# Kernel optimization log

Hardware: AMD Instinct MI355X
Metric: run time of the kernel (lower is better)

The kernel has to match this reference:

```python
import jax, jax.numpy as jnp
import numpy as np

MODES = 2
LC = 4
N = 6000
KNN = 10
NODES = 64
CH = MODES ** 2
M = N * 2 * (KNN + 1)  # total candidate couplings


def setup_inputs() -> dict:
    key = jax.random.key(0)
    ks = jax.random.split(key, 6)
    return {
        "CK_inputs": jax.random.normal(ks[0], (N, 2 * (KNN + 1), 3), dtype=jnp.float32),
        "W_in": jax.random.normal(ks[1], (3, NODES), dtype=jnp.float32) * 0.1,
        "b_in": jnp.zeros((NODES,), dtype=jnp.float32),
        "W_hid": jax.random.normal(ks[2], (LC - 1, NODES, NODES), dtype=jnp.float32) * 0.1,
        "b_hid": jnp.zeros((LC - 1, NODES), dtype=jnp.float32),
        "W_out": jax.random.normal(ks[3], (NODES, CH), dtype=jnp.float32) * 0.1,
        "b_out": jnp.zeros((CH,), dtype=jnp.float32),
        "coo": jax.random.randint(ks[4], (2, M), 0, N, dtype=jnp.int32),
    }


def _mlp(x, W_in, b_in, W_hid, b_hid, W_out, b_out):
    # MLP: 3 -> 64, (LC-1) hidden 64->64 layers, 64 -> CH; ReLU activations.
    h = jax.nn.relu(x @ W_in + b_in)
    for i in range(W_hid.shape[0]):  # small fixed layer count
        h = jax.nn.relu(h @ W_hid[i] + b_hid[i])
    return h @ W_out + b_out  # [M, CH]


def reference(CK_inputs, W_in, b_in, W_hid, b_hid, W_out, b_out, coo):
    C_stripped = _mlp(CK_inputs.reshape(-1, 3), W_in, b_in, W_hid, b_hid, W_out, b_out)  # [M, CH]
    D = MODES * N
    # Original: for channel ch = mi*MODES+mj, scatter C_stripped[:, ch] at indices coo*MODES+mj
    # (mj added to BOTH row and col, replicating the source exactly). Indices are
    # independent of mi, so sum over mi first, then one scatter-add per mj.
    vals = C_stripped.reshape(-1, MODES, MODES).sum(axis=1)  # [M, MODES]; axis1=mi, axis2=mj
    dense = jnp.zeros((D, D), dtype=CK_inputs.dtype)
    for mj in range(MODES):
        idx = coo * MODES + mj  # [2, M]
        dense = dense.at[idx[0], idx[1]].add(vals[:, mj])
    return dense
```

## Files before the change

### kernel.cpp

```cpp
#include <hip/hip_runtime.h>
#include <stdint.h>

#define NN    6000
#define KNNC  10
#define MM    (NN * 2 * (KNNC + 1))
#define DD    (2 * NN)
#define LCH   3
#define BLK   256

#define FBLOCKS ((MM + 63) / 64)
#define NV      ((long long)DD * DD / 4)

__global__ __launch_bounds__(BLK) void fused_mlp_zero(
    const float* __restrict__ CK,
    const float* __restrict__ Win,
    const float* __restrict__ bin,
    const float* __restrict__ Whid,
    const float* __restrict__ bhid,
    const float* __restrict__ Wout,
    const float* __restrict__ bout,
    float* __restrict__ vals,
    float* __restrict__ out)
{
    const int tid  = threadIdx.x;
    const int wave = tid >> 6;
    const int lane = tid & 63;
    const int mlpw = blockIdx.x & 3;

    if (wave != mlpw) {
        const int fw = wave - (wave > mlpw ? 1 : 0);
        const long long ft = (long long)blockIdx.x * 192 + fw * 64 + lane;
        const long long stride = (long long)FBLOCKS * 192;
        float4 z = make_float4(0.f, 0.f, 0.f, 0.f);
        float4* outv = (float4*)out;
        for (long long i = ft; i < NV; i += stride) outv[i] = z;
        return;
    }

    const int m = blockIdx.x * 64 + lane;
    if (m >= MM) return;

    const float x0 = CK[m * 3 + 0];
    const float x1 = CK[m * 3 + 1];
    const float x2 = CK[m * 3 + 2];

    float h[64];
#pragma unroll
    for (int j = 0; j < 64; j++) {
        float a = bin[j];
        a = fmaf(x0, Win[j],       a);
        a = fmaf(x1, Win[64 + j],  a);
        a = fmaf(x2, Win[128 + j], a);
        h[j] = fmaxf(a, 0.0f);
    }

#pragma unroll 1
    for (int l = 0; l < LCH; l++) {
        const float4* __restrict__ W4 = (const float4*)(Whid + (l << 12));
        const float*  __restrict__ bh = bhid + (l << 6);
        float g[64];
#pragma unroll
        for (int j = 0; j < 64; j++) g[j] = bh[j];
#pragma unroll 8
        for (int k = 0; k < 64; k++) {
            const float hk = h[k];
            const float4* __restrict__ Wk = W4 + (k << 4);
#pragma unroll
            for (int j4 = 0; j4 < 16; j4++) {
                float4 w = Wk[j4];
                g[j4 * 4 + 0] = fmaf(w.x, hk, g[j4 * 4 + 0]);
                g[j4 * 4 + 1] = fmaf(w.y, hk, g[j4 * 4 + 1]);
                g[j4 * 4 + 2] = fmaf(w.z, hk, g[j4 * 4 + 2]);
                g[j4 * 4 + 3] = fmaf(w.w, hk, g[j4 * 4 + 3]);
            }
        }
#pragma unroll
        for (int j = 0; j < 64; j++) h[j] = fmaxf(g[j], 0.0f);
    }

    float v0 = bout[0] + bout[2];
    float v1 = bout[1] + bout[3];
#pragma unroll
    for (int k = 0; k < 64; k++) {
        float4 wo = *((const float4*)Wout + k);
        v0 = fmaf(h[k], wo.x + wo.z, v0);
        v1 = fmaf(h[k], wo.y + wo.w, v1);
    }
    vals[m * 2 + 0] = v0;
    vals[m * 2 + 1] = v1;
}

__global__ __launch_bounds__(BLK) void scatter_add(
    const float* __restrict__ vals,
    const int* __restrict__ coo,
    float* __restrict__ out)
{
    const int t = blockIdx.x * BLK + threadIdx.x;
    if (t >= MM) return;
    const int r2 = coo[t] * 2;
    const int c2 = coo[MM + t] * 2;
    const float v0 = vals[t * 2 + 0];
    const float v1 = vals[t * 2 + 1];
    const long long f0 = (long long)r2 * DD + c2;
    atomicAdd(out + f0, v0);
    atomicAdd(out + f0 + DD + 1, v1);
}

extern "C" void kernel_launch(void* const* d_in, const int* in_sizes, int n_in,
                              void* d_out, int out_size, void* d_ws, size_t ws_size,
                              hipStream_t stream) {
    const float* CK   = (const float*)d_in[0];
    const float* Win  = (const float*)d_in[1];
    const float* bin  = (const float*)d_in[2];
    const float* Whid = (const float*)d_in[3];
    const float* bhid = (const float*)d_in[4];
    const float* Wout = (const float*)d_in[5];
    const float* bout = (const float*)d_in[6];
    const int* coo    = (const int*)d_in[7];
    float* out        = (float*)d_out;
    float* vals       = (float*)d_ws;

    fused_mlp_zero<<<FBLOCKS, BLK, 0, stream>>>(
        CK, Win, bin, Whid, bhid, Wout, bout, vals, out);
    scatter_add<<<(MM + BLK - 1) / BLK, BLK, 0, stream>>>(vals, coo, out);
}
```

Measured before the change: 710.8 us.

## Split fused MLP/zero-fill kernel into separate fill, MLP and scatter launches

Replaces the fused kernel, in which one wave per block ran the MLP and three waves zero-filled the output, with a dedicated grid-stride fill kernel followed by a full-block MLP kernel. Every thread in the MLP kernel now evaluates a row instead of one wave in four, and the k-loop unroll is reduced from 8 to 2 to limit register pressure. The cost is that the fill and the MLP no longer overlap, and there is one more kernel launch.

```diff
diff --git a/kernel.cpp b/kernel.cpp
--- a/kernel.cpp
+++ b/kernel.cpp
@@ -8,10 +8,19 @@
 #define LCH   3
 #define BLK   256
 
-#define FBLOCKS ((MM + 63) / 64)
-#define NV      ((long long)DD * DD / 4)
+#define NV          ((long long)DD * DD / 4)
+#define FILL_BLOCKS 4096
+#define MLP_BLOCKS  ((MM + BLK - 1) / BLK)
 
-__global__ __launch_bounds__(BLK) void fused_mlp_zero(
+__global__ __launch_bounds__(BLK) void fill_out(float* __restrict__ out) {
+    float4 z = make_float4(0.f, 0.f, 0.f, 0.f);
+    float4* outv = (float4*)out;
+    long long i = (long long)blockIdx.x * BLK + threadIdx.x;
+    const long long stride = (long long)FILL_BLOCKS * BLK;
+    for (; i < NV; i += stride) outv[i] = z;
+}
+
+__global__ __launch_bounds__(BLK) void mlp(
     const float* __restrict__ CK,
     const float* __restrict__ Win,
     const float* __restrict__ bin,
@@ -19,25 +28,9 @@
     const float* __restrict__ bhid,
     const float* __restrict__ Wout,
     const float* __restrict__ bout,
-    float* __restrict__ vals,
-    float* __restrict__ out)
+    float* __restrict__ vals)
 {
-    const int tid  = threadIdx.x;
-    const int wave = tid >> 6;
-    const int lane = tid & 63;
-    const int mlpw = blockIdx.x & 3;
-
-    if (wave != mlpw) {
-        const int fw = wave - (wave > mlpw ? 1 : 0);
-        const long long ft = (long long)blockIdx.x * 192 + fw * 64 + lane;
-        const long long stride = (long long)FBLOCKS * 192;
-        float4 z = make_float4(0.f, 0.f, 0.f, 0.f);
-        float4* outv = (float4*)out;
-        for (long long i = ft; i < NV; i += stride) outv[i] = z;
-        return;
-    }
-
-    const int m = blockIdx.x * 64 + lane;
+    const int m = blockIdx.x * BLK + threadIdx.x;
     if (m >= MM) return;
 
     const float x0 = CK[m * 3 + 0];
@@ -61,7 +54,7 @@
         float g[64];
 #pragma unroll
         for (int j = 0; j < 64; j++) g[j] = bh[j];
-#pragma unroll 8
+#pragma unroll 2
         for (int k = 0; k < 64; k++) {
             const float hk = h[k];
             const float4* __restrict__ Wk = W4 + (k << 4);
@@ -120,7 +113,7 @@
     float* out        = (float*)d_out;
     float* vals       = (float*)d_ws;
 
-    fused_mlp_zero<<<FBLOCKS, BLK, 0, stream>>>(
-        CK, Win, bin, Whid, bhid, Wout, bout, vals, out);
-    scatter_add<<<(MM + BLK - 1) / BLK, BLK, 0, stream>>>(vals, coo, out);
+    fill_out<<<FILL_BLOCKS, BLK, 0, stream>>>(out);
+    mlp<<<MLP_BLOCKS, BLK, 0, stream>>>(CK, Win, bin, Whid, bhid, Wout, bout, vals);
+    scatter_add<<<MLP_BLOCKS, BLK, 0, stream>>>(vals, coo, out);
 }
```

Result: slower. 746.6 us (+5.0%).
